# Optimization experiments

Hardware: AMD Instinct MI355X
Metric: run time of the kernel (lower is better)

Reference implementation:

```python
import jax, jax.numpy as jnp
import numpy as np
from jax import lax

SEQ, BATCH, IN, HID, OUT = 28, 8192, 28, 128, 10


def _lstm_layer(x, W_ih, W_hh, b_ih, b_hh):
    # x: [T, B, in]; PyTorch gate order: i, f, g, o
    # precompute input projection once (keeps scan body memory-bound on h only)
    xproj = jnp.einsum('tbi,gi->tbg', x, W_ih) + b_ih + b_hh  # [T, B, 4H]
    H = W_hh.shape[1]
    B = x.shape[1]
    h0 = jnp.zeros((B, H), x.dtype)
    c0 = jnp.zeros((B, H), x.dtype)

    def step(carry, xp_t):
        h, c = carry
        gates = xp_t + h @ W_hh.T  # [B, 4H]
        i, f, g, o = jnp.split(gates, 4, axis=-1)
        i = jax.nn.sigmoid(i)
        f = jax.nn.sigmoid(f)
        g = jnp.tanh(g)
        o = jax.nn.sigmoid(o)
        c = f * c + i * g
        h = o * jnp.tanh(c)
        return (h, c), h

    _, ys = lax.scan(step, (h0, c0), xproj)
    return ys  # [T, B, H]


def setup_inputs() -> dict:
    key = jax.random.key(0)
    ks = jax.random.split(key, 11)
    s_in = 1.0 / np.sqrt(HID)
    u = lambda k, shape: jax.random.uniform(k, shape, jnp.float32, -s_in, s_in)
    return {
        'X': jax.random.normal(ks[0], (SEQ, BATCH, IN), jnp.float32),
        'W_ih0': u(ks[1], (4 * HID, IN)),
        'W_hh0': u(ks[2], (4 * HID, HID)),
        'b_ih0': u(ks[3], (4 * HID,)),
        'b_hh0': u(ks[4], (4 * HID,)),
        'W_ih1': u(ks[5], (4 * HID, HID)),
        'W_hh1': u(ks[6], (4 * HID, HID)),
        'b_ih1': u(ks[7], (4 * HID,)),
        'b_hh1': u(ks[8], (4 * HID,)),
        'W_lin': u(ks[9], (OUT, HID)),
        'b_lin': u(ks[10], (OUT,)),
    }


def reference(X, W_ih0, W_hh0, b_ih0, b_hh0, W_ih1, W_hh1, b_ih1, b_hh1, W_lin, b_lin):
    h1 = _lstm_layer(X, W_ih0, W_hh0, b_ih0, b_hh0)   # [T, B, 128]
    h2 = _lstm_layer(h1, W_ih1, W_hh1, b_ih1, b_hh1)  # [T, B, 128]
    pred = h2[-1] @ W_lin.T + b_lin                   # [B, 10]
    return pred
```

## Files before the change

### kernel.cpp

```cpp
#include <hip/hip_runtime.h>
#include <hip/hip_bf16.h>

#define SEQ   28
#define BATCH 8192
#define NIN   28
#define HID   128
#define NOUT  10

#define SCL_SIG  (-1.4426950408889634f)
#define SCL_TANH (2.8853900817779268f)

typedef __bf16 bf16_t;
typedef __bf16 bf16x8 __attribute__((ext_vector_type(8)));
typedef float  f32x4  __attribute__((ext_vector_type(4)));

__device__ __forceinline__ unsigned swz(unsigned row, unsigned byte_in_row) {
    return row * 256u + (byte_in_row ^ ((row & 7u) << 4));
}

__device__ __forceinline__ void barrier_lds() {
    asm volatile("s_waitcnt lgkmcnt(0)\n\ts_barrier" ::: "memory");
}

__global__ void pack_w_kernel(const float* __restrict__ Whh0, bf16_t* __restrict__ o0,
                              const float* __restrict__ Whh1, bf16_t* __restrict__ o1,
                              const float* __restrict__ Wih1, bf16_t* __restrict__ o2) {
    int idx = blockIdx.x * 256 + threadIdx.x;
    int mi = idx >> 16;
    int e  = idx & 65535;
    const float* W = (mi == 0) ? Whh0 : (mi == 1) ? Whh1 : Wih1;
    bf16_t*      o = (mi == 0) ? o0   : (mi == 1) ? o1   : o2;
    int j    = e & 7;
    int frag = e >> 3;
    int lane = frag & 63;
    int ksnt = frag >> 6;
    int nt = ksnt & 31, ks = ksnt >> 5;
    int gate = nt * 16 + (lane & 15);
    int k    = ks * 32 + ((lane >> 4) << 3) + j;
    float s  = ((gate >> 7) == 2) ? SCL_TANH : SCL_SIG;
    o[e] = (bf16_t)(W[gate * 128 + k] * s);
}

__device__ __forceinline__ bf16x8 load_x0(const float* __restrict__ X,
                                          int t, int rb, int m, int l15, int l4) {
    const float* base = X + ((size_t)(t * BATCH + rb + 16 * m + l15)) * NIN + l4 * 8;
    f32x4 lo = *(const f32x4*)base;
    f32x4 hi = {0.f, 0.f, 0.f, 0.f};
    if (l4 < 3) hi = *(const f32x4*)(base + 4);
    bf16x8 v;
    #pragma unroll
    for (int j = 0; j < 4; ++j) { v[j] = (bf16_t)lo[j]; v[4 + j] = (bf16_t)hi[j]; }
    return v;
}

template <int LAYER>
__device__ __forceinline__ void lstm_step(
    int t, int tload, int rb, int tid, int lane, int w, int l15, int l4,
    unsigned char* smem,
    const float* __restrict__ X, const bf16_t* __restrict__ h1r,
    bf16_t* __restrict__ h1w,
    bf16x8 (&whh)[4][4], bf16x8 (&wih)[4][4],
    float (&bias)[4], float (&c)[2][4],
    bf16x8 (&xc)[4][2], bf16x8 (&xl)[4][2])
{
    constexpr int KS = (LAYER == 0) ? 1 : 4;
    unsigned char* hb = smem + ((t & 1) << 13);
    unsigned char* hn = smem + ((~t & 1) << 13);

    bf16x8 ah[4][2];
    #pragma unroll
    for (int ks = 0; ks < 4; ++ks)
        #pragma unroll
        for (int m = 0; m < 2; ++m)
            ah[ks][m] = *(const bf16x8*)(hb + swz(16 * m + l15, (ks * 32 + l4 * 8) * 2));

    f32x4 acc[2][4];
    #pragma unroll
    for (int m = 0; m < 2; ++m)
        #pragma unroll
        for (int q = 0; q < 4; ++q) {
            f32x4 b = {bias[q], bias[q], bias[q], bias[q]};
            acc[m][q] = b;
        }

    #pragma unroll
    for (int m = 0; m < 2; ++m)
        #pragma unroll
        for (int q = 0; q < 4; ++q)
            #pragma unroll
            for (int ks = 0; ks < KS; ++ks)
                acc[m][q] = __builtin_amdgcn_mfma_f32_16x16x32_bf16(
                    xc[ks][m], wih[q][ks], acc[m][q], 0, 0, 0);

    if (tload < SEQ) {
        if constexpr (LAYER == 0) {
            #pragma unroll
            for (int m = 0; m < 2; ++m)
                xl[0][m] = load_x0(X, tload, rb, m, l15, l4);
        } else {
            #pragma unroll
            for (int ks = 0; ks < 4; ++ks)
                #pragma unroll
                for (int m = 0; m < 2; ++m)
                    xl[ks][m] = *(const bf16x8*)(h1r + ((size_t)(tload * BATCH + rb + 16 * m + l15)) * HID + ks * 32 + l4 * 8);
        }
    }

    #pragma unroll
    for (int m = 0; m < 2; ++m)
        #pragma unroll
        for (int q = 0; q < 4; ++q)
            #pragma unroll
            for (int ks = 0; ks < 4; ++ks)
                acc[m][q] = __builtin_amdgcn_mfma_f32_16x16x32_bf16(
                    ah[ks][m], whh[q][ks], acc[m][q], 0, 0, 0);

    #pragma unroll
    for (int m = 0; m < 2; ++m)
        #pragma unroll
        for (int r = 0; r < 4; ++r) {
            float Ei = __builtin_amdgcn_exp2f(acc[m][0][r]);
            float Ef = __builtin_amdgcn_exp2f(acc[m][1][r]);
            float Eg = __builtin_amdgcn_exp2f(acc[m][2][r]);
            float Eo = __builtin_amdgcn_exp2f(acc[m][3][r]);
            float ti = 1.0f + Ei, tf = 1.0f + Ef;
            float tg = 1.0f + Eg, to = 1.0f + Eo;
            float titg = ti * tg;
            float num  = fmaf(c[m][r], titg, tf * (tg - 2.0f));
            float cn   = num * __builtin_amdgcn_rcpf(tf * titg);
            c[m][r] = cn;
            float Ec = __builtin_amdgcn_exp2f(SCL_TANH * cn);
            float hv = (Ec - 1.0f) * __builtin_amdgcn_rcpf(to * (1.0f + Ec));
            *(bf16_t*)(hn + swz(16 * m + l4 * 4 + r, (16 * w + l15) * 2)) = (bf16_t)hv;
        }
    barrier_lds();

    if constexpr (LAYER == 0) {
        int row = tid >> 4, sc = tid & 15;
        f32x4 v = *(const f32x4*)(hn + swz(row, sc * 16));
        *(f32x4*)((unsigned char*)h1w + ((size_t)(t * BATCH + rb + row)) * 256 + sc * 16) = v;
    }
}

__global__ __launch_bounds__(512, 2)
void lstm_fused_kernel(const float* __restrict__ Wih0,
                       const float* __restrict__ bih0, const float* __restrict__ bhh0,
                       const float* __restrict__ bih1, const float* __restrict__ bhh1,
                       const float* __restrict__ X,
                       const bf16_t* __restrict__ whhp0,
                       const bf16_t* __restrict__ whhp1,
                       const bf16_t* __restrict__ wihp1,
                       bf16_t* __restrict__ h1,
                       const float* __restrict__ Wlin, const float* __restrict__ blin,
                       float* __restrict__ out)
{
    __shared__ unsigned char smem[16384] __attribute__((aligned(16)));

    const int tid  = threadIdx.x;
    const int lane = tid & 63;
    const int w    = tid >> 6;
    const int l15  = lane & 15;
    const int l4   = lane >> 4;
    const int rb   = blockIdx.x * 32;

    bf16x8 whh[4][4], wih[4][4];
    float  bias[4];
    float  c[2][4];
    bf16x8 xA[4][2], xB[4][2];

    #pragma unroll
    for (int q = 0; q < 4; ++q)
        #pragma unroll
        for (int ks = 0; ks < 4; ++ks)
            whh[q][ks] = *(const bf16x8*)(whhp0 + ((size_t)((ks * 32 + (w + 8 * q)) * 64 + lane)) * 8);
    #pragma unroll
    for (int q = 0; q < 4; ++q) {
        int gate = 16 * w + 128 * q + l15;
        float s = (q == 2) ? SCL_TANH : SCL_SIG;
        #pragma unroll
        for (int j = 0; j < 8; ++j) {
            int k = l4 * 8 + j;
            wih[q][0][j] = (k < NIN) ? (bf16_t)(Wih0[gate * NIN + k] * s) : (bf16_t)0.0f;
        }
        bias[q] = (bih0[gate] + bhh0[gate]) * s;
        c[0][q] = 0.f; c[1][q] = 0.f;
    }
    for (int i = tid * 16; i < 16384; i += 512 * 16) {
        f32x4 z = {0.f, 0.f, 0.f, 0.f};
        *(f32x4*)(smem + i) = z;
    }
    #pragma unroll
    for (int m = 0; m < 2; ++m) {
        xA[0][m] = load_x0(X, 0, rb, m, l15, l4);
        xB[0][m] = load_x0(X, 1, rb, m, l15, l4);
    }
    __syncthreads();

    for (int t = 0; t < SEQ; t += 2) {
        lstm_step<0>(t,     t + 2, rb, tid, lane, w, l15, l4, smem, X, nullptr, h1,
                     whh, wih, bias, c, xA, xA);
        lstm_step<0>(t + 1, t + 3, rb, tid, lane, w, l15, l4, smem, X, nullptr, h1,
                     whh, wih, bias, c, xB, xB);
    }

    __syncthreads();

    #pragma unroll
    for (int q = 0; q < 4; ++q) {
        #pragma unroll
        for (int ks = 0; ks < 4; ++ks) {
            whh[q][ks] = *(const bf16x8*)(whhp1 + ((size_t)((ks * 32 + (w + 8 * q)) * 64 + lane)) * 8);
            wih[q][ks] = *(const bf16x8*)(wihp1 + ((size_t)((ks * 32 + (w + 8 * q)) * 64 + lane)) * 8);
        }
        int gate = 16 * w + 128 * q + l15;
        float s = (q == 2) ? SCL_TANH : SCL_SIG;
        bias[q] = (bih1[gate] + bhh1[gate]) * s;
        c[0][q] = 0.f; c[1][q] = 0.f;
    }
    for (int i = tid * 16; i < 16384; i += 512 * 16) {
        f32x4 z = {0.f, 0.f, 0.f, 0.f};
        *(f32x4*)(smem + i) = z;
    }
    #pragma unroll
    for (int ks = 0; ks < 4; ++ks)
        #pragma unroll
        for (int m = 0; m < 2; ++m)
            xA[ks][m] = *(const bf16x8*)(h1 + ((size_t)(rb + 16 * m + l15)) * HID + ks * 32 + l4 * 8);
    __syncthreads();

    for (int t = 0; t < SEQ; ++t)
        lstm_step<1>(t, t + 1, rb, tid, lane, w, l15, l4, smem, nullptr, h1, nullptr,
                     whh, wih, bias, c, xA, xA);

    if (tid < 32 * NOUT) {
        int row = tid / NOUT, oc = tid % NOUT;
        const unsigned char* hf = smem;
        float s = blin[oc];
        #pragma unroll 8
        for (int k = 0; k < HID; ++k) {
            float h = (float)*(const bf16_t*)(hf + swz(row, k * 2));
            s += h * Wlin[oc * HID + k];
        }
        out[(size_t)(rb + row) * NOUT + oc] = s;
    }
}

extern "C" void kernel_launch(void* const* d_in, const int* in_sizes, int n_in,
                              void* d_out, int out_size, void* d_ws, size_t ws_size,
                              hipStream_t stream) {
    const float* X    = (const float*)d_in[0];
    const float* Wih0 = (const float*)d_in[1];
    const float* Whh0 = (const float*)d_in[2];
    const float* bih0 = (const float*)d_in[3];
    const float* bhh0 = (const float*)d_in[4];
    const float* Wih1 = (const float*)d_in[5];
    const float* Whh1 = (const float*)d_in[6];
    const float* bih1 = (const float*)d_in[7];
    const float* bhh1 = (const float*)d_in[8];
    const float* Wlin = (const float*)d_in[9];
    const float* blin = (const float*)d_in[10];
    float* out = (float*)d_out;

    unsigned char* ws = (unsigned char*)d_ws;
    bf16_t* h1    = (bf16_t*)(ws);
    bf16_t* whhp0 = (bf16_t*)(ws + 58720256);
    bf16_t* whhp1 = (bf16_t*)(ws + 58851328);
    bf16_t* wihp1 = (bf16_t*)(ws + 58982400);

    pack_w_kernel<<<dim3(768), dim3(256), 0, stream>>>(Whh0, whhp0, Whh1, whhp1, Wih1, wihp1);

    lstm_fused_kernel<<<dim3(256), dim3(512), 0, stream>>>(
        Wih0, bih0, bhh0, bih1, bhh1, X, whhp0, whhp1, wihp1, h1,
        Wlin, blin, out);
}
```

Before: 133.1 us.

## Wavefront-pipeline both LSTM layers in one time loop with Whh0 in LDS

Interleaves layer 0 step s with layer 1 step s-1 in a single loop, so layer 1 reads layer-0 hidden state straight from LDS and the h1 sequence is no longer written to and read back from global memory. To free registers for both layers' weights, the layer-0 recurrent weights move into a 128KB LDS region and are read every step, while the layer-1 weights stay in registers. The loop now runs 29 barrier-separated steps instead of 56, but LDS use grows to about 152KB per block, which cuts occupancy and adds LDS bandwidth pressure.

```diff
diff --git a/kernel.cpp b/kernel.cpp
--- a/kernel.cpp
+++ b/kernel.cpp
@@ -53,108 +53,146 @@
     return v;
 }
 
-template <int LAYER>
-__device__ __forceinline__ void lstm_step(
-    int t, int tload, int rb, int tid, int lane, int w, int l15, int l4,
+__device__ __forceinline__ void act_store(f32x4 (&z)[4], f32x4& c,
+                                          unsigned char* buf, int rowbase, int colb)
+{
+    f32x4 Ei, Ef, Eg, Eo;
+    #pragma unroll
+    for (int r = 0; r < 4; ++r) {
+        Ei[r] = __builtin_amdgcn_exp2f(z[0][r]);
+        Ef[r] = __builtin_amdgcn_exp2f(z[1][r]);
+        Eg[r] = __builtin_amdgcn_exp2f(z[2][r]);
+        Eo[r] = __builtin_amdgcn_exp2f(z[3][r]);
+    }
+    f32x4 ti = Ei + 1.0f, tf = Ef + 1.0f;
+    f32x4 tg = Eg + 1.0f, to = Eo + 1.0f;
+    f32x4 titg = ti * tg;
+    f32x4 num  = c * titg + tf * (tg - 2.0f);
+    f32x4 den  = tf * titg;
+    f32x4 rif;
+    #pragma unroll
+    for (int r = 0; r < 4; ++r) rif[r] = __builtin_amdgcn_rcpf(den[r]);
+    f32x4 cn = num * rif;
+    c = cn;
+    f32x4 e2 = cn * SCL_TANH;
+    f32x4 Ec;
+    #pragma unroll
+    for (int r = 0; r < 4; ++r) Ec[r] = __builtin_amdgcn_exp2f(e2[r]);
+    f32x4 dh = to * (Ec + 1.0f);
+    f32x4 rh;
+    #pragma unroll
+    for (int r = 0; r < 4; ++r) rh[r] = __builtin_amdgcn_rcpf(dh[r]);
+    f32x4 hvf = (Ec - 1.0f) * rh;
+    #pragma unroll
+    for (int r = 0; r < 4; ++r)
+        *(bf16_t*)(buf + swz(rowbase + r, colb)) = (bf16_t)hvf[r];
+}
+
+#define OFF_H0 131072
+#define OFF_H2 147456
+
+template <int PAR, bool DO_L0, bool DO_L1>
+__device__ __forceinline__ void step_pipe(
+    int s, int rb, int tid, int w, int l15, int l4,
     unsigned char* smem,
-    const float* __restrict__ X, const bf16_t* __restrict__ h1r,
-    bf16_t* __restrict__ h1w,
-    bf16x8 (&whh)[4][4], bf16x8 (&wih)[4][4],
-    float (&bias)[4], float (&c)[2][4],
-    bf16x8 (&xc)[4][2], bf16x8 (&xl)[4][2])
+    const float* __restrict__ X,
+    bf16x8 (&wih0)[4],
+    bf16x8 (&whh1)[4][4], bf16x8 (&wih1)[4][4],
+    float (&bias0)[4], float (&bias1)[4],
+    f32x4 (&c0)[2], f32x4 (&c1)[2],
+    bf16x8 (&x0)[2])
 {
-    constexpr int KS = (LAYER == 0) ? 1 : 4;
-    unsigned char* hb = smem + ((t & 1) << 13);
-    unsigned char* hn = smem + ((~t & 1) << 13);
-
-    bf16x8 ah[4][2];
-    #pragma unroll
-    for (int ks = 0; ks < 4; ++ks)
-        #pragma unroll
-        for (int m = 0; m < 2; ++m)
-            ah[ks][m] = *(const bf16x8*)(hb + swz(16 * m + l15, (ks * 32 + l4 * 8) * 2));
-
-    f32x4 acc[2][4];
-    #pragma unroll
-    for (int m = 0; m < 2; ++m)
-        #pragma unroll
-        for (int q = 0; q < 4; ++q) {
-            f32x4 b = {bias[q], bias[q], bias[q], bias[q]};
-            acc[m][q] = b;
-        }
-
-    #pragma unroll
-    for (int m = 0; m < 2; ++m)
-        #pragma unroll
-        for (int q = 0; q < 4; ++q)
-            #pragma unroll
-            for (int ks = 0; ks < KS; ++ks)
-                acc[m][q] = __builtin_amdgcn_mfma_f32_16x16x32_bf16(
-                    xc[ks][m], wih[q][ks], acc[m][q], 0, 0, 0);
-
-    if (tload < SEQ) {
-        if constexpr (LAYER == 0) {
-            #pragma unroll
-            for (int m = 0; m < 2; ++m)
-                xl[0][m] = load_x0(X, tload, rb, m, l15, l4);
-        } else {
-            #pragma unroll
-            for (int ks = 0; ks < 4; ++ks)
+    unsigned char* h0r = smem + OFF_H0 + ((PAR ^ 1) << 13);
+    unsigned char* h0w = smem + OFF_H0 + (PAR << 13);
+    unsigned char* h2b = smem + OFF_H2;
+    const int colb = (16 * w + l15) * 2;
+
+    barrier_lds();
+
+    if constexpr (DO_L1) {
+        f32x4 acc1[2][4];
+        #pragma unroll
+        for (int m = 0; m < 2; ++m)
+            #pragma unroll
+            for (int q = 0; q < 4; ++q) {
+                f32x4 b = {bias1[q], bias1[q], bias1[q], bias1[q]};
+                acc1[m][q] = b;
+            }
+        #pragma unroll
+        for (int ks = 0; ks < 4; ++ks) {
+            bf16x8 hA[2], h2A[2];
+            #pragma unroll
+            for (int m = 0; m < 2; ++m) {
+                hA[m]  = *(const bf16x8*)(h0r + swz(16 * m + l15, (ks * 32 + l4 * 8) * 2));
+                h2A[m] = *(const bf16x8*)(h2b + swz(16 * m + l15, (ks * 32 + l4 * 8) * 2));
+            }
+            #pragma unroll
+            for (int m = 0; m < 2; ++m)
                 #pragma unroll
-                for (int m = 0; m < 2; ++m)
-                    xl[ks][m] = *(const bf16x8*)(h1r + ((size_t)(tload * BATCH + rb + 16 * m + l15)) * HID + ks * 32 + l4 * 8);
-        }
-    }
-
-    #pragma unroll
-    for (int m = 0; m < 2; ++m)
-        #pragma unroll
-        for (int q = 0; q < 4; ++q)
-            #pragma unroll
-            for (int ks = 0; ks < 4; ++ks)
-                acc[m][q] = __builtin_amdgcn_mfma_f32_16x16x32_bf16(
-                    ah[ks][m], whh[q][ks], acc[m][q], 0, 0, 0);
-
-    #pragma unroll
-    for (int m = 0; m < 2; ++m)
-        #pragma unroll
-        for (int r = 0; r < 4; ++r) {
-            float Ei = __builtin_amdgcn_exp2f(acc[m][0][r]);
-            float Ef = __builtin_amdgcn_exp2f(acc[m][1][r]);
-            float Eg = __builtin_amdgcn_exp2f(acc[m][2][r]);
-            float Eo = __builtin_amdgcn_exp2f(acc[m][3][r]);
-            float ti = 1.0f + Ei, tf = 1.0f + Ef;
-            float tg = 1.0f + Eg, to = 1.0f + Eo;
-            float titg = ti * tg;
-            float num  = fmaf(c[m][r], titg, tf * (tg - 2.0f));
-            float cn   = num * __builtin_amdgcn_rcpf(tf * titg);
-            c[m][r] = cn;
-            float Ec = __builtin_amdgcn_exp2f(SCL_TANH * cn);
-            float hv = (Ec - 1.0f) * __builtin_amdgcn_rcpf(to * (1.0f + Ec));
-            *(bf16_t*)(hn + swz(16 * m + l4 * 4 + r, (16 * w + l15) * 2)) = (bf16_t)hv;
-        }
-    barrier_lds();
-
-    if constexpr (LAYER == 0) {
-        int row = tid >> 4, sc = tid & 15;
-        f32x4 v = *(const f32x4*)(hn + swz(row, sc * 16));
-        *(f32x4*)((unsigned char*)h1w + ((size_t)(t * BATCH + rb + row)) * 256 + sc * 16) = v;
+                for (int q = 0; q < 4; ++q) {
+                    acc1[m][q] = __builtin_amdgcn_mfma_f32_16x16x32_bf16(
+                        hA[m], wih1[q][ks], acc1[m][q], 0, 0, 0);
+                    acc1[m][q] = __builtin_amdgcn_mfma_f32_16x16x32_bf16(
+                        h2A[m], whh1[q][ks], acc1[m][q], 0, 0, 0);
+                }
+        }
+        barrier_lds();
+        #pragma unroll
+        for (int m = 0; m < 2; ++m)
+            act_store(acc1[m], c1[m], h2b, 16 * m + l4 * 4, colb);
+    }
+
+    if constexpr (DO_L0) {
+        f32x4 acc0[2][4];
+        #pragma unroll
+        for (int m = 0; m < 2; ++m)
+            #pragma unroll
+            for (int q = 0; q < 4; ++q) {
+                f32x4 b = {bias0[q], bias0[q], bias0[q], bias0[q]};
+                acc0[m][q] = __builtin_amdgcn_mfma_f32_16x16x32_bf16(
+                    x0[m], wih0[q], b, 0, 0, 0);
+            }
+        #pragma unroll
+        for (int ks = 0; ks < 4; ++ks) {
+            bf16x8 hA[2];
+            #pragma unroll
+            for (int m = 0; m < 2; ++m)
+                hA[m] = *(const bf16x8*)(h0r + swz(16 * m + l15, (ks * 32 + l4 * 8) * 2));
+            bf16x8 wB[4];
+            #pragma unroll
+            for (int q = 0; q < 4; ++q)
+                wB[q] = *(const bf16x8*)(smem + ((unsigned)((ks * 32 + (w + 8 * q)) * 64 + (tid & 63))) * 16u);
+            #pragma unroll
+            for (int m = 0; m < 2; ++m)
+                #pragma unroll
+                for (int q = 0; q < 4; ++q)
+                    acc0[m][q] = __builtin_amdgcn_mfma_f32_16x16x32_bf16(
+                        hA[m], wB[q], acc0[m][q], 0, 0, 0);
+        }
+        #pragma unroll
+        for (int m = 0; m < 2; ++m)
+            act_store(acc0[m], c0[m], h0w, 16 * m + l4 * 4, colb);
+
+        if (s + 1 < SEQ) {
+            #pragma unroll
+            for (int m = 0; m < 2; ++m)
+                x0[m] = load_x0(X, s + 1, rb, m, l15, l4);
+        }
     }
 }
 
 __global__ __launch_bounds__(512, 2)
-void lstm_fused_kernel(const float* __restrict__ Wih0,
-                       const float* __restrict__ bih0, const float* __restrict__ bhh0,
-                       const float* __restrict__ bih1, const float* __restrict__ bhh1,
-                       const float* __restrict__ X,
-                       const bf16_t* __restrict__ whhp0,
-                       const bf16_t* __restrict__ whhp1,
-                       const bf16_t* __restrict__ wihp1,
-                       bf16_t* __restrict__ h1,
-                       const float* __restrict__ Wlin, const float* __restrict__ blin,
-                       float* __restrict__ out)
+void lstm_pipe_kernel(const float* __restrict__ Wih0,
+                      const float* __restrict__ bih0, const float* __restrict__ bhh0,
+                      const float* __restrict__ bih1, const float* __restrict__ bhh1,
+                      const float* __restrict__ X,
+                      const bf16_t* __restrict__ whhp0,
+                      const bf16_t* __restrict__ whhp1,
+                      const bf16_t* __restrict__ wihp1,
+                      const float* __restrict__ Wlin, const float* __restrict__ blin,
+                      float* __restrict__ out)
 {
-    __shared__ unsigned char smem[16384] __attribute__((aligned(16)));
+    __shared__ unsigned char smem[155648] __attribute__((aligned(16)));
 
     const int tid  = threadIdx.x;
     const int lane = tid & 63;
@@ -163,16 +201,24 @@
     const int l4   = lane >> 4;
     const int rb   = blockIdx.x * 32;
 
-    bf16x8 whh[4][4], wih[4][4];
-    float  bias[4];
-    float  c[2][4];
-    bf16x8 xA[4][2], xB[4][2];
-
+    bf16x8 wih0[4], whh1[4][4], wih1[4][4];
+    float  bias0[4], bias1[4];
+    f32x4  c0[2], c1[2];
+    bf16x8 x0[2];
+
+    for (int i = tid * 16; i < 131072; i += 512 * 16)
+        *(f32x4*)(smem + i) = *(const f32x4*)((const unsigned char*)whhp0 + i);
+    for (int i = tid * 16; i < 24576; i += 512 * 16) {
+        f32x4 z = {0.f, 0.f, 0.f, 0.f};
+        *(f32x4*)(smem + OFF_H0 + i) = z;
+    }
     #pragma unroll
     for (int q = 0; q < 4; ++q)
         #pragma unroll
-        for (int ks = 0; ks < 4; ++ks)
-            whh[q][ks] = *(const bf16x8*)(whhp0 + ((size_t)((ks * 32 + (w + 8 * q)) * 64 + lane)) * 8);
+        for (int ks = 0; ks < 4; ++ks) {
+            whh1[q][ks] = *(const bf16x8*)(whhp1 + ((size_t)((ks * 32 + (w + 8 * q)) * 64 + lane)) * 8);
+            wih1[q][ks] = *(const bf16x8*)(wihp1 + ((size_t)((ks * 32 + (w + 8 * q)) * 64 + lane)) * 8);
+        }
     #pragma unroll
     for (int q = 0; q < 4; ++q) {
         int gate = 16 * w + 128 * q + l15;
@@ -180,61 +226,38 @@
         #pragma unroll
         for (int j = 0; j < 8; ++j) {
             int k = l4 * 8 + j;
-            wih[q][0][j] = (k < NIN) ? (bf16_t)(Wih0[gate * NIN + k] * s) : (bf16_t)0.0f;
-        }
-        bias[q] = (bih0[gate] + bhh0[gate]) * s;
-        c[0][q] = 0.f; c[1][q] = 0.f;
-    }
-    for (int i = tid * 16; i < 16384; i += 512 * 16) {
+            wih0[q][j] = (k < NIN) ? (bf16_t)(Wih0[gate * NIN + k] * s) : (bf16_t)0.0f;
+        }
+        bias0[q] = (bih0[gate] + bhh0[gate]) * s;
+        bias1[q] = (bih1[gate] + bhh1[gate]) * s;
+    }
+    {
         f32x4 z = {0.f, 0.f, 0.f, 0.f};
-        *(f32x4*)(smem + i) = z;
-    }
-    #pragma unroll
-    for (int m = 0; m < 2; ++m) {
-        xA[0][m] = load_x0(X, 0, rb, m, l15, l4);
-        xB[0][m] = load_x0(X, 1, rb, m, l15, l4);
-    }
+        c0[0] = z; c0[1] = z; c1[0] = z; c1[1] = z;
+    }
+    #pragma unroll
+    for (int m = 0; m < 2; ++m)
+        x0[m] = load_x0(X, 0, rb, m, l15, l4);
     __syncthreads();
 
-    for (int t = 0; t < SEQ; t += 2) {
-        lstm_step<0>(t,     t + 2, rb, tid, lane, w, l15, l4, smem, X, nullptr, h1,
-                     whh, wih, bias, c, xA, xA);
-        lstm_step<0>(t + 1, t + 3, rb, tid, lane, w, l15, l4, smem, X, nullptr, h1,
-                     whh, wih, bias, c, xB, xB);
-    }
-
-    __syncthreads();
-
-    #pragma unroll
-    for (int q = 0; q < 4; ++q) {
-        #pragma unroll
-        for (int ks = 0; ks < 4; ++ks) {
-            whh[q][ks] = *(const bf16x8*)(whhp1 + ((size_t)((ks * 32 + (w + 8 * q)) * 64 + lane)) * 8);
-            wih[q][ks] = *(const bf16x8*)(wihp1 + ((size_t)((ks * 32 + (w + 8 * q)) * 64 + lane)) * 8);
-        }
-        int gate = 16 * w + 128 * q + l15;
-        float s = (q == 2) ? SCL_TANH : SCL_SIG;
-        bias[q] = (bih1[gate] + bhh1[gate]) * s;
-        c[0][q] = 0.f; c[1][q] = 0.f;
-    }
-    for (int i = tid * 16; i < 16384; i += 512 * 16) {
-        f32x4 z = {0.f, 0.f, 0.f, 0.f};
-        *(f32x4*)(smem + i) = z;
-    }
-    #pragma unroll
-    for (int ks = 0; ks < 4; ++ks)
-        #pragma unroll
-        for (int m = 0; m < 2; ++m)
-            xA[ks][m] = *(const bf16x8*)(h1 + ((size_t)(rb + 16 * m + l15)) * HID + ks * 32 + l4 * 8);
-    __syncthreads();
-
-    for (int t = 0; t < SEQ; ++t)
-        lstm_step<1>(t, t + 1, rb, tid, lane, w, l15, l4, smem, nullptr, h1, nullptr,
-                     whh, wih, bias, c, xA, xA);
+    step_pipe<0, true, false>(0, rb, tid, w, l15, l4, smem, X,
+                              wih0, whh1, wih1, bias0, bias1, c0, c1, x0);
+    for (int s = 1; s <= 25; s += 2) {
+        step_pipe<1, true, true>(s,     rb, tid, w, l15, l4, smem, X,
+                                 wih0, whh1, wih1, bias0, bias1, c0, c1, x0);
+        step_pipe<0, true, true>(s + 1, rb, tid, w, l15, l4, smem, X,
+                                 wih0, whh1, wih1, bias0, bias1, c0, c1, x0);
+    }
+    step_pipe<1, true,  true>(27, rb, tid, w, l15, l4, smem, X,
+                              wih0, whh1, wih1, bias0, bias1, c0, c1, x0);
+    step_pipe<0, false, true>(28, rb, tid, w, l15, l4, smem, X,
+                              wih0, whh1, wih1, bias0, bias1, c0, c1, x0);
+
+    barrier_lds();
 
     if (tid < 32 * NOUT) {
         int row = tid / NOUT, oc = tid % NOUT;
-        const unsigned char* hf = smem;
+        const unsigned char* hf = smem + OFF_H2;
         float s = blin[oc];
         #pragma unroll 8
         for (int k = 0; k < HID; ++k) {
@@ -262,14 +285,13 @@
     float* out = (float*)d_out;
 
     unsigned char* ws = (unsigned char*)d_ws;
-    bf16_t* h1    = (bf16_t*)(ws);
-    bf16_t* whhp0 = (bf16_t*)(ws + 58720256);
-    bf16_t* whhp1 = (bf16_t*)(ws + 58851328);
-    bf16_t* wihp1 = (bf16_t*)(ws + 58982400);
+    bf16_t* whhp0 = (bf16_t*)(ws);
+    bf16_t* whhp1 = (bf16_t*)(ws + 131072);
+    bf16_t* wihp1 = (bf16_t*)(ws + 262144);
 
     pack_w_kernel<<<dim3(768), dim3(256), 0, stream>>>(Whh0, whhp0, Whh1, whhp1, Wih1, wihp1);
 
-    lstm_fused_kernel<<<dim3(256), dim3(512), 0, stream>>>(
-        Wih0, bih0, bhh0, bih1, bhh1, X, whhp0, whhp1, wihp1, h1,
+    lstm_pipe_kernel<<<dim3(256), dim3(512), 0, stream>>>(
+        Wih0, bih0, bhh0, bih1, bhh1, X, whhp0, whhp1, wihp1,
         Wlin, blin, out);
 }
```

New measurement: 335.8 us. +152.2%, slower.
